# Kernel optimization log

Hardware: AMD Instinct MI355X
Metric: run time of the kernel (lower is better)

Reference implementation:

```python
import jax, jax.numpy as jnp
import numpy as np

B, E, H, KVH, S = 1, 4096, 32, 8, 2048
HD = E // H            # per-head dim = 128
KVE = KVH * HD         # kv projection embed dim = 1024


def setup_inputs() -> dict:
    key = jax.random.key(0)
    ks = jax.random.split(key, 10)
    std = 0.02
    return {
        "input_embeds": jax.random.normal(ks[0], (B, E, 1, S), jnp.float32),
        "cos": jax.random.uniform(ks[1], (HD, S), jnp.float32, -1.0, 1.0),
        "sin": jax.random.uniform(ks[2], (HD, S), jnp.float32, -1.0, 1.0),
        "wq": jax.random.normal(ks[3], (E, E), jnp.float32) * std,
        "bq": jnp.zeros((E,), jnp.float32),
        "wk": jax.random.normal(ks[4], (KVE, E), jnp.float32) * std,
        "wv": jax.random.normal(ks[5], (KVE, E), jnp.float32) * std,
        "bv": jnp.zeros((KVE,), jnp.float32),
        "wo": jax.random.normal(ks[6], (E, E), jnp.float32) * std,
        "bo": jnp.zeros((E,), jnp.float32),
    }


def _proj(w, x, b=None):
    # 1x1 Conv2d == channelwise linear on (B, C, 1, S)
    y = jnp.einsum('oc,bcxs->boxs', w, x)
    if b is not None:
        y = y + b[None, :, None, None]
    return y


def _rope(x, cos, sin):
    # x: (B, h, HD, S); rotate-half along head_dim axis
    half = x.shape[2] // 2
    x1, x2 = x[:, :, :half], x[:, :, half:]
    rot = jnp.concatenate([-x2, x1], axis=2)
    return x * cos[None, None] + rot * sin[None, None]


def reference(input_embeds, cos, sin, wq, bq, wk, wv, bv, wo, bo):
    b, e, _, s = input_embeds.shape
    hd = e // H
    q = _proj(wq, input_embeds, bq)          # (B, E, 1, S)
    k = _proj(wk, input_embeds)              # (B, KVE, 1, S)  (no bias)
    v = _proj(wv, input_embeds, bv)          # (B, KVE, 1, S)

    qh = q.reshape(b, H, hd, s)
    kh = k.reshape(b, KVH, hd, s)
    qh = _rope(qh, cos, sin)
    kh = _rope(kh, cos, sin)

    # GQA tiling: channel-block repeat => query head h uses kv head (h % KVH)
    rep = H // KVH
    kfull = jnp.tile(kh, (1, rep, 1, 1))                       # (B, H, HD, S)
    vfull = jnp.tile(v.reshape(b, KVH, hd, s), (1, rep, 1, 1))  # (B, H, HD, S)

    scale = 1.0 / np.sqrt(hd).astype(np.float32)
    scores = jnp.einsum('bhcq,bhck->bhqk', qh, kfull) * scale  # (B, H, S, S)
    causal = jnp.tril(jnp.ones((s, s), bool))
    scores = jnp.where(causal[None, None], scores, jnp.finfo(scores.dtype).min)
    w = jax.nn.softmax(scores, axis=-1)
    attn = jnp.einsum('bhqk,bhck->bhcq', w, vfull).reshape(b, e, 1, s)
    return _proj(wo, attn, bo)
```

## Files before the change

### kernel.cpp

```cpp
#include <hip/hip_runtime.h>


typedef unsigned short u16;
typedef unsigned int u32;
typedef __attribute__((ext_vector_type(8))) short bf16x8;
typedef __attribute__((ext_vector_type(4))) float f32x4;

__device__ __forceinline__ u16 f2b(float f){
  union { float f; u32 u; } v; v.f = f;
  u32 r = (v.u + 0x7FFFu + ((v.u >> 16) & 1u)) >> 16;
  return (u16)r;
}
__device__ __forceinline__ float b2f(u16 b){
  union { u32 u; float f; } v; v.u = ((u32)b) << 16;
  return v.f;
}

__device__ __forceinline__ void gld16(const void* g, void* l){
  __builtin_amdgcn_global_load_lds((const __attribute__((address_space(1))) u32*)g,
                                   (__attribute__((address_space(3))) u32*)l, 16, 0, 0);
}

__global__ __launch_bounds__(256) void cvt_w(const float* __restrict__ src,
                                             u16* __restrict__ dst, int n4)
{
  int i = blockIdx.x * 256 + threadIdx.x;
  if (i < n4){
    float4 v = *(const float4*)&src[(size_t)i * 4];
    ushort4 o; o.x = f2b(v.x); o.y = f2b(v.y); o.z = f2b(v.z); o.w = f2b(v.w);
    *(ushort4*)&dst[(size_t)i * 4] = o;
  }
}

__global__ __launch_bounds__(256) void transpose_x(const float* __restrict__ X,
                                                   u16* __restrict__ XT)
{
  __shared__ float lds[64][65];
  const int c0 = blockIdx.x * 64, s0 = blockIdx.y * 64;
  const int tid = threadIdx.x;
  {
    const int sg = tid & 15, cl = tid >> 4;
#pragma unroll
    for (int p = 0; p < 4; ++p){
      int c = cl + p * 16;
      float4 v = *(const float4*)&X[(size_t)(c0 + c) * 2048 + s0 + sg * 4];
      lds[sg*4+0][c] = v.x; lds[sg*4+1][c] = v.y;
      lds[sg*4+2][c] = v.z; lds[sg*4+3][c] = v.w;
    }
  }
  __syncthreads();
  {
    const int cg = tid & 15, sl = tid >> 4;
#pragma unroll
    for (int p = 0; p < 4; ++p){
      int s = sl + p * 16;
      ushort4 o;
      o.x = f2b(lds[s][cg*4+0]); o.y = f2b(lds[s][cg*4+1]);
      o.z = f2b(lds[s][cg*4+2]); o.w = f2b(lds[s][cg*4+3]);
      *(ushort4*)&XT[(size_t)(s0 + s) * 4096 + c0 + cg * 4] = o;
    }
  }
}

template<int EPI, int ABF>
__global__ __launch_bounds__(256) void gemm2(
    const u16* __restrict__ W0, const u16* __restrict__ W1, const u16* __restrict__ W2,
    const float* __restrict__ F0, const float* __restrict__ F1, const float* __restrict__ F2,
    const u16* __restrict__ B,
    const float* __restrict__ bias0, const float* __restrict__ bias2,
    u16* __restrict__ QTo, u16* __restrict__ KTo, u16* __restrict__ Vno,
    float* __restrict__ OUT)
{
  const int K = 4096;
  const int m0 = blockIdx.y * 128, n0 = blockIdx.x * 128;

  const u16* A16; const float* Af; int mA;
  if (EPI == 0){
    if (m0 < 4096)      { A16 = W0; Af = F0; mA = m0; }
    else if (m0 < 5120) { A16 = W1; Af = F1; mA = m0 - 4096; }
    else                { A16 = W2; Af = F2; mA = m0 - 5120; }
  } else { A16 = W0; Af = F0; mA = m0; }

  __shared__ __align__(16) u16 As[128 * 32];
  __shared__ __align__(16) u16 Bs[128 * 32];

  const int tid = threadIdx.x, lane = tid & 63, w = tid >> 6;
  const int wm = w >> 1, wn = w & 1, quad = lane >> 4, l15 = lane & 15;

  f32x4 acc[4][4];
#pragma unroll
  for (int mt = 0; mt < 4; ++mt)
#pragma unroll
    for (int nt = 0; nt < 4; ++nt)
      acc[mt][nt] = f32x4{0.f, 0.f, 0.f, 0.f};

  const int r0 = tid >> 2, gs0 = tid & 3;
  const int g0 = gs0 ^ ((r0 >> 1) & 3);
  const int r1 = r0 + 64;

  u16* ldsA0 = As + (size_t)(w * 64) * 8;
  u16* ldsA1 = As + (size_t)(w * 64 + 256) * 8;
  u16* ldsB0 = Bs + (size_t)(w * 64) * 8;
  u16* ldsB1 = Bs + (size_t)(w * 64 + 256) * 8;

  const u16* bsrc0 = &B[(size_t)(n0 + r0) * 4096 + g0 * 8];
  const u16* bsrc1 = &B[(size_t)(n0 + r1) * 4096 + g0 * 8];
  const u16* asrc0 = ABF ? &A16[(size_t)(mA + r0) * 4096 + g0 * 8] : nullptr;
  const u16* asrc1 = ABF ? &A16[(size_t)(mA + r1) * 4096 + g0 * 8] : nullptr;
  const float* afs0 = ABF ? nullptr : &Af[(size_t)(mA + r0) * 4096 + g0 * 8];
  const float* afs1 = ABF ? nullptr : &Af[(size_t)(mA + r1) * 4096 + g0 * 8];

  int aoff[4], boff[4];
#pragma unroll
  for (int mt = 0; mt < 4; ++mt){
    int row = wm * 64 + mt * 16 + l15;
    aoff[mt] = row * 32 + (quad ^ ((row >> 1) & 3)) * 8;
  }
#pragma unroll
  for (int nt = 0; nt < 4; ++nt){
    int row = wn * 64 + nt * 16 + l15;
    boff[nt] = row * 32 + (quad ^ ((row >> 1) & 3)) * 8;
  }

  for (int kt = 0; kt < K / 32; ++kt){
    const int k0 = kt * 32;
    if (ABF){
      gld16(asrc0 + k0, ldsA0);
      gld16(asrc1 + k0, ldsA1);
    } else {
      float4 v0 = *(const float4*)&afs0[k0];
      float4 v1 = *(const float4*)&afs0[k0 + 4];
      float4 v2 = *(const float4*)&afs1[k0];
      float4 v3 = *(const float4*)&afs1[k0 + 4];
      union { u16 u[8]; uint4 q; } p0, p1;
      p0.u[0]=f2b(v0.x); p0.u[1]=f2b(v0.y); p0.u[2]=f2b(v0.z); p0.u[3]=f2b(v0.w);
      p0.u[4]=f2b(v1.x); p0.u[5]=f2b(v1.y); p0.u[6]=f2b(v1.z); p0.u[7]=f2b(v1.w);
      p1.u[0]=f2b(v2.x); p1.u[1]=f2b(v2.y); p1.u[2]=f2b(v2.z); p1.u[3]=f2b(v2.w);
      p1.u[4]=f2b(v3.x); p1.u[5]=f2b(v3.y); p1.u[6]=f2b(v3.z); p1.u[7]=f2b(v3.w);
      *(uint4*)&As[(size_t)tid * 8] = p0.q;
      *(uint4*)&As[(size_t)(tid + 256) * 8] = p1.q;
    }
    gld16(bsrc0 + k0, ldsB0);
    gld16(bsrc1 + k0, ldsB1);
    __syncthreads();

    bf16x8 af[4], bfr[4];
#pragma unroll
    for (int mt = 0; mt < 4; ++mt) af[mt]  = *(const bf16x8*)&As[aoff[mt]];
#pragma unroll
    for (int nt = 0; nt < 4; ++nt) bfr[nt] = *(const bf16x8*)&Bs[boff[nt]];
#pragma unroll
    for (int mt = 0; mt < 4; ++mt)
#pragma unroll
      for (int nt = 0; nt < 4; ++nt)
        acc[mt][nt] = __builtin_amdgcn_mfma_f32_16x16x32_bf16(af[mt], bfr[nt], acc[mt][nt], 0, 0, 0);
    __syncthreads();
  }

  if (EPI == 0){
    if (m0 < 4096){
#pragma unroll
      for (int mt = 0; mt < 4; ++mt){
        int mb = m0 + wm * 64 + mt * 16 + quad * 4;
        float b0 = bias0[mb], b1 = bias0[mb+1], b2 = bias0[mb+2], b3 = bias0[mb+3];
#pragma unroll
        for (int nt = 0; nt < 4; ++nt){
          int n = n0 + wn * 64 + nt * 16 + l15;
          ushort4 o;
          o.x = f2b(acc[mt][nt][0] + b0); o.y = f2b(acc[mt][nt][1] + b1);
          o.z = f2b(acc[mt][nt][2] + b2); o.w = f2b(acc[mt][nt][3] + b3);
          *(ushort4*)&QTo[(size_t)n * 4096 + mb] = o;
        }
      }
    } else if (m0 < 5120){
#pragma unroll
      for (int mt = 0; mt < 4; ++mt){
        int mb = m0 - 4096 + wm * 64 + mt * 16 + quad * 4;
#pragma unroll
        for (int nt = 0; nt < 4; ++nt){
          int n = n0 + wn * 64 + nt * 16 + l15;
          ushort4 o;
          o.x = f2b(acc[mt][nt][0]); o.y = f2b(acc[mt][nt][1]);
          o.z = f2b(acc[mt][nt][2]); o.w = f2b(acc[mt][nt][3]);
          *(ushort4*)&KTo[(size_t)n * 1024 + mb] = o;
        }
      }
    } else {
#pragma unroll
      for (int mt = 0; mt < 4; ++mt)
#pragma unroll
        for (int r = 0; r < 4; ++r){
          int mv = m0 - 5120 + wm * 64 + mt * 16 + quad * 4 + r;
          float bb = bias2[mv];
#pragma unroll
          for (int nt = 0; nt < 4; ++nt){
            int n = n0 + wn * 64 + nt * 16 + l15;
            Vno[(size_t)mv * 2048 + n] = f2b(acc[mt][nt][r] + bb);
          }
        }
    }
  } else {
#pragma unroll
    for (int mt = 0; mt < 4; ++mt)
#pragma unroll
      for (int r = 0; r < 4; ++r){
        int m = m0 + wm * 64 + mt * 16 + quad * 4 + r;
        float bb = bias0[m];
#pragma unroll
        for (int nt = 0; nt < 4; ++nt){
          int n = n0 + wn * 64 + nt * 16 + l15;
          OUT[(size_t)m * 2048 + n] = acc[mt][nt][r] + bb;
        }
      }
  }
}

template<int EPI>
__global__ __launch_bounds__(512, 2) void gemm256(
    const u16* __restrict__ W0, const u16* __restrict__ W1, const u16* __restrict__ W2,
    const u16* __restrict__ Bmat,
    const float* __restrict__ bias0, const float* __restrict__ bias2,
    u16* __restrict__ QTo, u16* __restrict__ KTo, u16* __restrict__ Vno,
    float* __restrict__ OUT)
{
  const int NT = 64;
  const int m0 = blockIdx.y * 256, n0 = blockIdx.x * 256;

  const u16* A16; int mA;
  if (EPI == 0){
    if (m0 < 4096)      { A16 = W0; mA = m0; }
    else if (m0 < 5120) { A16 = W1; mA = m0 - 4096; }
    else                { A16 = W2; mA = m0 - 5120; }
  } else { A16 = W0; mA = m0; }

  __shared__ __align__(16) u16 As[2 * 2 * 8192];
  __shared__ __align__(16) u16 Bs[2 * 2 * 8192];

  const int tid = threadIdx.x, lane = tid & 63, w = tid >> 6;
  const int wm = w >> 2, wn = w & 3, quad = lane >> 4, l15 = lane & 15;

  f32x4 acc[8][4];
#pragma unroll
  for (int mt = 0; mt < 8; ++mt)
#pragma unroll
    for (int nt = 0; nt < 4; ++nt)
      acc[mt][nt] = f32x4{0.f, 0.f, 0.f, 0.f};

  const int rowq = tid >> 2;
  const int kg   = (tid & 3) * 8;
  const u16* aG = &A16[(size_t)(mA + rowq) * 4096 + kg];
  const u16* bG = &Bmat[(size_t)(n0 + rowq) * 4096 + kg];
  u16* AsW = As + w * 512;
  u16* BsW = Bs + w * 512;

  int aoff[8], boff[4];
#pragma unroll
  for (int mt = 0; mt < 8; ++mt) aoff[mt] = (wm * 128 + mt * 16 + l15) * 32 + quad * 8;
#pragma unroll
  for (int nt = 0; nt < 4; ++nt) boff[nt] = (wn * 64 + nt * 16 + l15) * 32 + quad * 8;

  auto stage8 = [&](int b, int k0){
    u16* Ad = AsW + b * 16384;
    u16* Bd = BsW + b * 16384;
    const u16* as_ = aG + k0;
    const u16* bs_ = bG + k0;
    gld16(as_,                   Ad);
    gld16(as_ + 128 * 4096,      Ad + 4096);
    gld16(bs_,                   Bd);
    gld16(bs_ + 128 * 4096,      Bd + 4096);
    gld16(as_ + 32,              Ad + 8192);
    gld16(as_ + 32 + 128 * 4096, Ad + 8192 + 4096);
    gld16(bs_ + 32,              Bd + 8192);
    gld16(bs_ + 32 + 128 * 4096, Bd + 8192 + 4096);
  };

  stage8(0, 0);
  asm volatile("s_waitcnt vmcnt(4)" ::: "memory");
  __builtin_amdgcn_s_barrier();
  __builtin_amdgcn_sched_barrier(0);

#pragma unroll 1
  for (int t = 0; t < NT; ++t){
    const int buf = t & 1;
    const u16* Asl = As + buf * 16384;
    const u16* Bsl = Bs + buf * 16384;

    {
      bf16x8 af[8], bf[4];
#pragma unroll
      for (int mt = 0; mt < 8; ++mt) af[mt] = *(const bf16x8*)&Asl[aoff[mt]];
#pragma unroll
      for (int nt = 0; nt < 4; ++nt) bf[nt] = *(const bf16x8*)&Bsl[boff[nt]];
      if (t + 1 < NT) stage8((t + 1) & 1, (t + 1) * 64);
      __builtin_amdgcn_s_setprio(1);
#pragma unroll
      for (int mt = 0; mt < 8; ++mt)
#pragma unroll
        for (int nt = 0; nt < 4; ++nt)
          acc[mt][nt] = __builtin_amdgcn_mfma_f32_16x16x32_bf16(af[mt], bf[nt], acc[mt][nt], 0, 0, 0);
      __builtin_amdgcn_s_setprio(0);
      if (t + 1 < NT) { asm volatile("s_waitcnt vmcnt(8)" ::: "memory"); }
      else            { asm volatile("s_waitcnt vmcnt(0)" ::: "memory"); }
      __builtin_amdgcn_s_barrier();
      __builtin_amdgcn_sched_barrier(0);
    }
    {
      bf16x8 af[8], bf[4];
#pragma unroll
      for (int mt = 0; mt < 8; ++mt) af[mt] = *(const bf16x8*)&Asl[8192 + aoff[mt]];
#pragma unroll
      for (int nt = 0; nt < 4; ++nt) bf[nt] = *(const bf16x8*)&Bsl[8192 + boff[nt]];
      __builtin_amdgcn_s_setprio(1);
#pragma unroll
      for (int mt = 0; mt < 8; ++mt)
#pragma unroll
        for (int nt = 0; nt < 4; ++nt)
          acc[mt][nt] = __builtin_amdgcn_mfma_f32_16x16x32_bf16(af[mt], bf[nt], acc[mt][nt], 0, 0, 0);
      __builtin_amdgcn_s_setprio(0);
      if (t + 1 < NT) { asm volatile("s_waitcnt vmcnt(4)" ::: "memory"); }
      __builtin_amdgcn_s_barrier();
      __builtin_amdgcn_sched_barrier(0);
    }
  }

  if (EPI == 0){
    if (m0 < 4096){
#pragma unroll
      for (int mt = 0; mt < 8; ++mt){
        int mb = m0 + wm * 128 + mt * 16 + quad * 4;
        float b0 = bias0[mb], b1 = bias0[mb+1], b2 = bias0[mb+2], b3 = bias0[mb+3];
#pragma unroll
        for (int nt = 0; nt < 4; ++nt){
          int n = n0 + wn * 64 + nt * 16 + l15;
          ushort4 o;
          o.x = f2b(acc[mt][nt][0] + b0); o.y = f2b(acc[mt][nt][1] + b1);
          o.z = f2b(acc[mt][nt][2] + b2); o.w = f2b(acc[mt][nt][3] + b3);
          *(ushort4*)&QTo[(size_t)n * 4096 + mb] = o;
        }
      }
    } else if (m0 < 5120){
#pragma unroll
      for (int mt = 0; mt < 8; ++mt){
        int mb = m0 - 4096 + wm * 128 + mt * 16 + quad * 4;
#pragma unroll
        for (int nt = 0; nt < 4; ++nt){
          int n = n0 + wn * 64 + nt * 16 + l15;
          ushort4 o;
          o.x = f2b(acc[mt][nt][0]); o.y = f2b(acc[mt][nt][1]);
          o.z = f2b(acc[mt][nt][2]); o.w = f2b(acc[mt][nt][3]);
          *(ushort4*)&KTo[(size_t)n * 1024 + mb] = o;
        }
      }
    } else {
#pragma unroll
      for (int mt = 0; mt < 8; ++mt)
#pragma unroll
        for (int r = 0; r < 4; ++r){
          int mv = m0 - 5120 + wm * 128 + mt * 16 + quad * 4 + r;
          float bb = bias2[mv];
#pragma unroll
          for (int nt = 0; nt < 4; ++nt){
            int n = n0 + wn * 64 + nt * 16 + l15;
            Vno[(size_t)mv * 2048 + n] = f2b(acc[mt][nt][r] + bb);
          }
        }
    }
  } else {
#pragma unroll
    for (int mt = 0; mt < 8; ++mt)
#pragma unroll
      for (int r = 0; r < 4; ++r){
        int m = m0 + wm * 128 + mt * 16 + quad * 4 + r;
        float bb = bias0[m];
#pragma unroll
        for (int nt = 0; nt < 4; ++nt){
          int n = n0 + wn * 64 + nt * 16 + l15;
          OUT[(size_t)m * 2048 + n] = acc[mt][nt][r] + bb;
        }
      }
  }
}

__global__ __launch_bounds__(256) void rope_kernel(u16* __restrict__ QT,
                                                   u16* __restrict__ KT,
                                                   const float* __restrict__ cosp,
                                                   const float* __restrict__ sinp)
{
  const float qscale = 0.08838834764831845f * 1.4426950408889634f;
  int gid = blockIdx.x * 256 + threadIdx.x;
  const int NQ = 2048 * 32 * 64;
  if (gid < NQ){
    int c = gid & 63, hh = (gid >> 6) & 31, s = gid >> 11;
    size_t base = (size_t)s * 4096 + hh * 128 + c;
    float x1 = b2f(QT[base]), x2 = b2f(QT[base + 64]);
    float c1 = cosp[c * 2048 + s],        s1 = sinp[c * 2048 + s];
    float c2 = cosp[(c + 64) * 2048 + s], s2 = sinp[(c + 64) * 2048 + s];
    QT[base]      = f2b((x1 * c1 - x2 * s1) * qscale);
    QT[base + 64] = f2b((x2 * c2 + x1 * s2) * qscale);
  } else {
    int g = gid - NQ;
    int c = g & 63, hh = (g >> 6) & 7, s = g >> 9;
    size_t base = (size_t)s * 1024 + hh * 128 + c;
    float x1 = b2f(KT[base]), x2 = b2f(KT[base + 64]);
    float c1 = cosp[c * 2048 + s],        s1 = sinp[c * 2048 + s];
    float c2 = cosp[(c + 64) * 2048 + s], s2 = sinp[(c + 64) * 2048 + s];
    KT[base]      = f2b(x1 * c1 - x2 * s1);
    KT[base + 64] = f2b(x2 * c2 + x1 * s2);
  }
}

__global__ __launch_bounds__(256, 1) void attn3(const u16* __restrict__ QT,
                                                const u16* __restrict__ KT,
                                                const u16* __restrict__ Vn,
                                                u16* __restrict__ AT)
{
  const int h = blockIdx.x;
  const int p = blockIdx.y;
  const int kvh = h & 7;
  const int tid = threadIdx.x;
  const int w = tid >> 6, lane = tid & 63;
  const int quad = lane >> 4, l15 = lane & 15;

  const int k  = 4 * p + w;
  const int t1 = k, t2 = 63 - k;
  const int e1 = t1 >> 1, e2 = t2 >> 1;
  const int i01 = t1 * 32, i02 = t2 * 32;
  const int U = 32 - 2 * p;

  __shared__ __align__(16) u16 Ks[2][64 * 128];
  __shared__ __align__(16) u16 Vs[128 * 64];
  __shared__ __align__(16) u16 Ps[4][16][64];

  bf16x8 qa1[2][4], qa2[2][4];
#pragma unroll
  for (int mt = 0; mt < 2; ++mt)
#pragma unroll
    for (int kc = 0; kc < 4; ++kc){
      qa1[mt][kc] = *(const bf16x8*)&QT[(size_t)(i01 + mt * 16 + l15) * 4096
                                        + h * 128 + kc * 32 + quad * 8];
      qa2[mt][kc] = *(const bf16x8*)&QT[(size_t)(i02 + mt * 16 + l15) * 4096
                                        + h * 128 + kc * 32 + quad * 8];
    }

  f32x4 o1[2][9], o2[2][9];
#pragma unroll
  for (int mt = 0; mt < 2; ++mt)
#pragma unroll
    for (int ct = 0; ct < 9; ++ct){
      o1[mt][ct] = f32x4{0.f, 0.f, 0.f, 0.f};
      o2[mt][ct] = f32x4{0.f, 0.f, 0.f, 0.f};
    }

  bf16x8 ones;
#pragma unroll
  for (int z = 0; z < 8; ++z) ones[z] = (short)0x3F80;

  const int krl = lane >> 4, kgl = lane & 15;
  const int vrl = lane >> 3, vgl = lane & 7;

  auto stageK = [&](int buf, int j0){
#pragma unroll
    for (int q = 0; q < 4; ++q){
      int r = w * 16 + q * 4 + krl;
      gld16(&KT[(size_t)(j0 + r) * 1024 + kvh * 128 + ((kgl ^ (r & 7)) * 8)],
            &Ks[buf][(size_t)(w * 16 + q * 4) * 128]);
    }
  };
  auto stageV = [&](int j0){
#pragma unroll
    for (int q = 0; q < 4; ++q){
      int r = w * 32 + q * 8 + vrl;
      gld16(&Vn[(size_t)(kvh * 128 + r) * 2048 + j0 + ((vgl ^ (r & 7)) * 8)],
            &Vs[(size_t)(w * 32 + q * 8) * 64]);
    }
  };

  auto soft = [&](f32x4 (&s)[2][4], bf16x8 (&pa)[2][2], f32x4 (&o)[2][9],
                  int i0, int j0, bool maskit){
#pragma unroll
    for (int mt = 0; mt < 2; ++mt){
#pragma unroll
      for (int nt = 0; nt < 4; ++nt)
#pragma unroll
        for (int r = 0; r < 4; ++r){
          float pv = exp2f(fminf(s[mt][nt][r], 60.0f));
          if (maskit && (j0 + nt * 16 + l15 > i0 + mt * 16 + quad * 4 + r)) pv = 0.0f;
          int col = nt * 16 + l15, rowp = quad * 4 + r;
          Ps[w][rowp][((col >> 3) ^ (rowp & 7)) * 8 + (col & 7)] = f2b(pv);
        }
#pragma unroll
      for (int kc = 0; kc < 2; ++kc){
        pa[mt][kc] = *(const bf16x8*)&Ps[w][l15][((kc * 4 + quad) ^ (l15 & 7)) * 8];
        o[mt][8] = __builtin_amdgcn_mfma_f32_16x16x32_bf16(pa[mt][kc], ones, o[mt][8], 0, 0, 0);
      }
    }
  };

  auto epilogue = [&](f32x4 (&o)[2][9], int i0){
#pragma unroll
    for (int mt = 0; mt < 2; ++mt){
      float rinv[4];
#pragma unroll
      for (int r = 0; r < 4; ++r) rinv[r] = 1.0f / o[mt][8][r];
#pragma unroll
      for (int ct = 0; ct < 8; ++ct)
#pragma unroll
        for (int r = 0; r < 4; ++r){
          int i = i0 + mt * 16 + quad * 4 + r;
          AT[(size_t)i * 4096 + h * 128 + ct * 16 + l15] = f2b(o[mt][ct][r] * rinv[r]);
        }
    }
  };

  stageK(0, 0);
  for (int u = 0; u < U; ++u){
    __syncthreads();
    if (u + 1 < U) stageK((u + 1) & 1, (u + 1) * 64);
    stageV(u * 64);

    const int j0 = u * 64;
    const bool act1 = (u <= e1), act2 = (u <= e2);
    const u16* Kb = &Ks[u & 1][0];

    f32x4 s1[2][4], s2[2][4];
    bf16x8 pa1[2][2], pa2[2][2];
    if (act2 || act1){
#pragma unroll
      for (int mt = 0; mt < 2; ++mt)
#pragma unroll
        for (int nt = 0; nt < 4; ++nt){
          s1[mt][nt] = f32x4{0.f, 0.f, 0.f, 0.f};
          s2[mt][nt] = f32x4{0.f, 0.f, 0.f, 0.f};
        }
#pragma unroll
      for (int nt = 0; nt < 4; ++nt){
        bf16x8 kb[4];
#pragma unroll
        for (int kc = 0; kc < 4; ++kc){
          int row = nt * 16 + l15;
          kb[kc] = *(const bf16x8*)&Kb[row * 128 + (((kc * 4 + quad) ^ (row & 7)) * 8)];
        }
#pragma unroll
        for (int kc = 0; kc < 4; ++kc){
          s2[0][nt] = __builtin_amdgcn_mfma_f32_16x16x32_bf16(qa2[0][kc], kb[kc], s2[0][nt], 0, 0, 0);
          s2[1][nt] = __builtin_amdgcn_mfma_f32_16x16x32_bf16(qa2[1][kc], kb[kc], s2[1][nt], 0, 0, 0);
        }
        if (act1)
#pragma unroll
          for (int kc = 0; kc < 4; ++kc){
            s1[0][nt] = __builtin_amdgcn_mfma_f32_16x16x32_bf16(qa1[0][kc], kb[kc], s1[0][nt], 0, 0, 0);
            s1[1][nt] = __builtin_amdgcn_mfma_f32_16x16x32_bf16(qa1[1][kc], kb[kc], s1[1][nt], 0, 0, 0);
          }
      }
      if (act2) soft(s2, pa2, o2, i02, j0, u == e2);
      if (act1) soft(s1, pa1, o1, i01, j0, u == e1);
    }
    __syncthreads();

    if (act2 || act1){
#pragma unroll
      for (int ct = 0; ct < 8; ++ct)
#pragma unroll
        for (int kc = 0; kc < 2; ++kc){
          int row = ct * 16 + l15;
          bf16x8 vb = *(const bf16x8*)&Vs[row * 64 + (((kc * 4 + quad) ^ (row & 7)) * 8)];
          if (act2){
            o2[0][ct] = __builtin_amdgcn_mfma_f32_16x16x32_bf16(pa2[0][kc], vb, o2[0][ct], 0, 0, 0);
            o2[1][ct] = __builtin_amdgcn_mfma_f32_16x16x32_bf16(pa2[1][kc], vb, o2[1][ct], 0, 0, 0);
          }
          if (act1){
            o1[0][ct] = __builtin_amdgcn_mfma_f32_16x16x32_bf16(pa1[0][kc], vb, o1[0][ct], 0, 0, 0);
            o1[1][ct] = __builtin_amdgcn_mfma_f32_16x16x32_bf16(pa1[1][kc], vb, o1[1][ct], 0, 0, 0);
          }
        }
      if (u == e2) epilogue(o2, i02);
      if (u == e1) epilogue(o1, i01);
    }
  }
}

extern "C" void kernel_launch(void* const* d_in, const int* in_sizes, int n_in,
                              void* d_out, int out_size, void* d_ws, size_t ws_size,
                              hipStream_t stream)
{
  const float* X    = (const float*)d_in[0];
  const float* cosp = (const float*)d_in[1];
  const float* sinp = (const float*)d_in[2];
  const float* wq   = (const float*)d_in[3];
  const float* bq   = (const float*)d_in[4];
  const float* wk   = (const float*)d_in[5];
  const float* wv   = (const float*)d_in[6];
  const float* bv   = (const float*)d_in[7];
  const float* wo   = (const float*)d_in[8];
  const float* bo   = (const float*)d_in[9];
  float* out = (float*)d_out;

  char* ws = (char*)d_ws;
  const size_t MB = 1u << 20;

  if (ws_size >= 88 * MB){
    u16* W16Q = (u16*)(ws);
    u16* W16K = (u16*)(ws + 32 * MB);
    u16* W16V = (u16*)(ws + 40 * MB);
    u16* XT   = (u16*)(ws + 48 * MB);
    u16* QT   = (u16*)(ws + 64 * MB);
    u16* KT   = (u16*)(ws + 80 * MB);
    u16* Vn   = (u16*)(ws + 84 * MB);
    u16* AT   = (u16*)(ws + 48 * MB);
    u16* WO16 = (u16*)(ws);

    cvt_w<<<16384, 256, 0, stream>>>(wq, W16Q, 4194304);
    cvt_w<<< 4096, 256, 0, stream>>>(wk, W16K, 1048576);
    cvt_w<<< 4096, 256, 0, stream>>>(wv, W16V, 1048576);
    transpose_x<<<dim3(64, 32), 256, 0, stream>>>(X, XT);
    gemm256<0><<<dim3(8, 24), 512, 0, stream>>>(W16Q, W16K, W16V, XT,
                                                bq, bv, QT, KT, Vn, nullptr);
    cvt_w<<<16384, 256, 0, stream>>>(wo, WO16, 4194304);
    rope_kernel<<<20480, 256, 0, stream>>>(QT, KT, cosp, sinp);
    attn3<<<dim3(32, 8), 256, 0, stream>>>(QT, KT, Vn, AT);
    gemm256<1><<<dim3(8, 16), 512, 0, stream>>>(WO16, nullptr, nullptr, AT,
                                                bo, nullptr, nullptr, nullptr, nullptr, out);
  } else {
    u16* XT = (u16*)(ws);
    u16* QT = (u16*)(ws + 16 * MB);
    u16* KT = (u16*)(ws + 32 * MB);
    u16* Vn = (u16*)(ws + 36 * MB);
    u16* AT = (u16*)(ws + 40 * MB);

    transpose_x<<<dim3(64, 32), 256, 0, stream>>>(X, XT);
    gemm2<0,0><<<dim3(16, 48), 256, 0, stream>>>(nullptr, nullptr, nullptr, wq, wk, wv,
                                                 XT, bq, bv, QT, KT, Vn, nullptr);
    rope_kernel<<<20480, 256, 0, stream>>>(QT, KT, cosp, sinp);
    attn3<<<dim3(32, 8), 256, 0, stream>>>(QT, KT, Vn, AT);
    gemm2<1,0><<<dim3(16, 32), 256, 0, stream>>>(nullptr, nullptr, nullptr, wo, nullptr, nullptr,
                                                 AT, bo, nullptr, nullptr, nullptr, nullptr, out);
  }
}
```

Before: 673.1 us.

## Split attention work so each wave owns one query tile, doubling grid

The causal attention kernel previously had each wave process two paired query tiles (t and 63-t) within 8 blocks per head. Now each block handles a pair of block-rows q and 15-q. Two waves take consecutive early tiles and two take consecutive late tiles, with one tile per wave, giving 512 blocks instead of 256. This raises occupancy and parallelism across the CUs and halves per-wave register state. In exchange, each K/V tile is staged by more blocks and waves within a block are less balanced.

```diff
diff --git a/kernel.cpp b/kernel.cpp
--- a/kernel.cpp
+++ b/kernel.cpp
@@ -409,47 +409,42 @@
   }
 }
 
-__global__ __launch_bounds__(256, 1) void attn3(const u16* __restrict__ QT,
+__global__ __launch_bounds__(256, 1) void attn4(const u16* __restrict__ QT,
                                                 const u16* __restrict__ KT,
                                                 const u16* __restrict__ Vn,
                                                 u16* __restrict__ AT)
 {
   const int h = blockIdx.x;
-  const int p = blockIdx.y;
+  const int Y = blockIdx.y;
+  const int q = (Y < 8) ? Y : 23 - Y;
   const int kvh = h & 7;
   const int tid = threadIdx.x;
   const int w = tid >> 6, lane = tid & 63;
   const int quad = lane >> 4, l15 = lane & 15;
 
-  const int k  = 4 * p + w;
-  const int t1 = k, t2 = 63 - k;
-  const int e1 = t1 >> 1, e2 = t2 >> 1;
-  const int i01 = t1 * 32, i02 = t2 * 32;
-  const int U = 32 - 2 * p;
+  const int t = (w < 2) ? (2 * q + w) : (62 - 2 * q + (w - 2));
+  const int e  = t >> 1;
+  const int i0 = t * 32;
+  const int U  = 32 - q;
 
   __shared__ __align__(16) u16 Ks[2][64 * 128];
   __shared__ __align__(16) u16 Vs[128 * 64];
   __shared__ __align__(16) u16 Ps[4][16][64];
 
-  bf16x8 qa1[2][4], qa2[2][4];
+  bf16x8 qa[2][4];
 #pragma unroll
   for (int mt = 0; mt < 2; ++mt)
 #pragma unroll
-    for (int kc = 0; kc < 4; ++kc){
-      qa1[mt][kc] = *(const bf16x8*)&QT[(size_t)(i01 + mt * 16 + l15) * 4096
-                                        + h * 128 + kc * 32 + quad * 8];
-      qa2[mt][kc] = *(const bf16x8*)&QT[(size_t)(i02 + mt * 16 + l15) * 4096
-                                        + h * 128 + kc * 32 + quad * 8];
-    }
-
-  f32x4 o1[2][9], o2[2][9];
+    for (int kc = 0; kc < 4; ++kc)
+      qa[mt][kc] = *(const bf16x8*)&QT[(size_t)(i0 + mt * 16 + l15) * 4096
+                                       + h * 128 + kc * 32 + quad * 8];
+
+  f32x4 o[2][9];
 #pragma unroll
   for (int mt = 0; mt < 2; ++mt)
 #pragma unroll
-    for (int ct = 0; ct < 9; ++ct){
-      o1[mt][ct] = f32x4{0.f, 0.f, 0.f, 0.f};
-      o2[mt][ct] = f32x4{0.f, 0.f, 0.f, 0.f};
-    }
+    for (int ct = 0; ct < 9; ++ct)
+      o[mt][ct] = f32x4{0.f, 0.f, 0.f, 0.f};
 
   bf16x8 ones;
 #pragma unroll
@@ -460,55 +455,18 @@
 
   auto stageK = [&](int buf, int j0){
 #pragma unroll
-    for (int q = 0; q < 4; ++q){
-      int r = w * 16 + q * 4 + krl;
+    for (int qq = 0; qq < 4; ++qq){
+      int r = w * 16 + qq * 4 + krl;
       gld16(&KT[(size_t)(j0 + r) * 1024 + kvh * 128 + ((kgl ^ (r & 7)) * 8)],
-            &Ks[buf][(size_t)(w * 16 + q * 4) * 128]);
+            &Ks[buf][(size_t)(w * 16 + qq * 4) * 128]);
     }
   };
   auto stageV = [&](int j0){
 #pragma unroll
-    for (int q = 0; q < 4; ++q){
-      int r = w * 32 + q * 8 + vrl;
+    for (int qq = 0; qq < 4; ++qq){
+      int r = w * 32 + qq * 8 + vrl;
       gld16(&Vn[(size_t)(kvh * 128 + r) * 2048 + j0 + ((vgl ^ (r & 7)) * 8)],
-            &Vs[(size_t)(w * 32 + q * 8) * 64]);
-    }
-  };
-
-  auto soft = [&](f32x4 (&s)[2][4], bf16x8 (&pa)[2][2], f32x4 (&o)[2][9],
-                  int i0, int j0, bool maskit){
-#pragma unroll
-    for (int mt = 0; mt < 2; ++mt){
-#pragma unroll
-      for (int nt = 0; nt < 4; ++nt)
-#pragma unroll
-        for (int r = 0; r < 4; ++r){
-          float pv = exp2f(fminf(s[mt][nt][r], 60.0f));
-          if (maskit && (j0 + nt * 16 + l15 > i0 + mt * 16 + quad * 4 + r)) pv = 0.0f;
-          int col = nt * 16 + l15, rowp = quad * 4 + r;
-          Ps[w][rowp][((col >> 3) ^ (rowp & 7)) * 8 + (col & 7)] = f2b(pv);
-        }
-#pragma unroll
-      for (int kc = 0; kc < 2; ++kc){
-        pa[mt][kc] = *(const bf16x8*)&Ps[w][l15][((kc * 4 + quad) ^ (l15 & 7)) * 8];
-        o[mt][8] = __builtin_amdgcn_mfma_f32_16x16x32_bf16(pa[mt][kc], ones, o[mt][8], 0, 0, 0);
-      }
-    }
-  };
-
-  auto epilogue = [&](f32x4 (&o)[2][9], int i0){
-#pragma unroll
-    for (int mt = 0; mt < 2; ++mt){
-      float rinv[4];
-#pragma unroll
-      for (int r = 0; r < 4; ++r) rinv[r] = 1.0f / o[mt][8][r];
-#pragma unroll
-      for (int ct = 0; ct < 8; ++ct)
-#pragma unroll
-        for (int r = 0; r < 4; ++r){
-          int i = i0 + mt * 16 + quad * 4 + r;
-          AT[(size_t)i * 4096 + h * 128 + ct * 16 + l15] = f2b(o[mt][ct][r] * rinv[r]);
-        }
+            &Vs[(size_t)(w * 32 + qq * 8) * 64]);
     }
   };
 
@@ -519,19 +477,17 @@
     stageV(u * 64);
 
     const int j0 = u * 64;
-    const bool act1 = (u <= e1), act2 = (u <= e2);
+    const bool act = (u <= e);
     const u16* Kb = &Ks[u & 1][0];
 
-    f32x4 s1[2][4], s2[2][4];
-    bf16x8 pa1[2][2], pa2[2][2];
-    if (act2 || act1){
+    f32x4 s[2][4];
+    bf16x8 pa[2][2];
+    if (act){
 #pragma unroll
       for (int mt = 0; mt < 2; ++mt)
 #pragma unroll
-        for (int nt = 0; nt < 4; ++nt){
-          s1[mt][nt] = f32x4{0.f, 0.f, 0.f, 0.f};
-          s2[mt][nt] = f32x4{0.f, 0.f, 0.f, 0.f};
-        }
+        for (int nt = 0; nt < 4; ++nt)
+          s[mt][nt] = f32x4{0.f, 0.f, 0.f, 0.f};
 #pragma unroll
       for (int nt = 0; nt < 4; ++nt){
         bf16x8 kb[4];
@@ -542,39 +498,56 @@
         }
 #pragma unroll
         for (int kc = 0; kc < 4; ++kc){
-          s2[0][nt] = __builtin_amdgcn_mfma_f32_16x16x32_bf16(qa2[0][kc], kb[kc], s2[0][nt], 0, 0, 0);
-          s2[1][nt] = __builtin_amdgcn_mfma_f32_16x16x32_bf16(qa2[1][kc], kb[kc], s2[1][nt], 0, 0, 0);
-        }
-        if (act1)
-#pragma unroll
-          for (int kc = 0; kc < 4; ++kc){
-            s1[0][nt] = __builtin_amdgcn_mfma_f32_16x16x32_bf16(qa1[0][kc], kb[kc], s1[0][nt], 0, 0, 0);
-            s1[1][nt] = __builtin_amdgcn_mfma_f32_16x16x32_bf16(qa1[1][kc], kb[kc], s1[1][nt], 0, 0, 0);
+          s[0][nt] = __builtin_amdgcn_mfma_f32_16x16x32_bf16(qa[0][kc], kb[kc], s[0][nt], 0, 0, 0);
+          s[1][nt] = __builtin_amdgcn_mfma_f32_16x16x32_bf16(qa[1][kc], kb[kc], s[1][nt], 0, 0, 0);
+        }
+      }
+      const bool maskit = (u == e);
+#pragma unroll
+      for (int mt = 0; mt < 2; ++mt){
+#pragma unroll
+        for (int nt = 0; nt < 4; ++nt)
+#pragma unroll
+          for (int r = 0; r < 4; ++r){
+            float pv = exp2f(fminf(s[mt][nt][r], 60.0f));
+            if (maskit && (j0 + nt * 16 + l15 > i0 + mt * 16 + quad * 4 + r)) pv = 0.0f;
+            int col = nt * 16 + l15, rowp = quad * 4 + r;
+            Ps[w][rowp][((col >> 3) ^ (rowp & 7)) * 8 + (col & 7)] = f2b(pv);
           }
-      }
-      if (act2) soft(s2, pa2, o2, i02, j0, u == e2);
-      if (act1) soft(s1, pa1, o1, i01, j0, u == e1);
+#pragma unroll
+        for (int kc = 0; kc < 2; ++kc){
+          pa[mt][kc] = *(const bf16x8*)&Ps[w][l15][((kc * 4 + quad) ^ (l15 & 7)) * 8];
+          o[mt][8] = __builtin_amdgcn_mfma_f32_16x16x32_bf16(pa[mt][kc], ones, o[mt][8], 0, 0, 0);
+        }
+      }
     }
     __syncthreads();
 
-    if (act2 || act1){
+    if (act){
 #pragma unroll
       for (int ct = 0; ct < 8; ++ct)
 #pragma unroll
         for (int kc = 0; kc < 2; ++kc){
           int row = ct * 16 + l15;
           bf16x8 vb = *(const bf16x8*)&Vs[row * 64 + (((kc * 4 + quad) ^ (row & 7)) * 8)];
-          if (act2){
-            o2[0][ct] = __builtin_amdgcn_mfma_f32_16x16x32_bf16(pa2[0][kc], vb, o2[0][ct], 0, 0, 0);
-            o2[1][ct] = __builtin_amdgcn_mfma_f32_16x16x32_bf16(pa2[1][kc], vb, o2[1][ct], 0, 0, 0);
-          }
-          if (act1){
-            o1[0][ct] = __builtin_amdgcn_mfma_f32_16x16x32_bf16(pa1[0][kc], vb, o1[0][ct], 0, 0, 0);
-            o1[1][ct] = __builtin_amdgcn_mfma_f32_16x16x32_bf16(pa1[1][kc], vb, o1[1][ct], 0, 0, 0);
-          }
-        }
-      if (u == e2) epilogue(o2, i02);
-      if (u == e1) epilogue(o1, i01);
+          o[0][ct] = __builtin_amdgcn_mfma_f32_16x16x32_bf16(pa[0][kc], vb, o[0][ct], 0, 0, 0);
+          o[1][ct] = __builtin_amdgcn_mfma_f32_16x16x32_bf16(pa[1][kc], vb, o[1][ct], 0, 0, 0);
+        }
+      if (u == e){
+#pragma unroll
+        for (int mt = 0; mt < 2; ++mt){
+          float rinv[4];
+#pragma unroll
+          for (int r = 0; r < 4; ++r) rinv[r] = 1.0f / o[mt][8][r];
+#pragma unroll
+          for (int ct = 0; ct < 8; ++ct)
+#pragma unroll
+            for (int r = 0; r < 4; ++r){
+              int i = i0 + mt * 16 + quad * 4 + r;
+              AT[(size_t)i * 4096 + h * 128 + ct * 16 + l15] = f2b(o[mt][ct][r] * rinv[r]);
+            }
+        }
+      }
     }
   }
 }
@@ -617,7 +590,7 @@
                                                 bq, bv, QT, KT, Vn, nullptr);
     cvt_w<<<16384, 256, 0, stream>>>(wo, WO16, 4194304);
     rope_kernel<<<20480, 256, 0, stream>>>(QT, KT, cosp, sinp);
-    attn3<<<dim3(32, 8), 256, 0, stream>>>(QT, KT, Vn, AT);
+    attn4<<<dim3(32, 16), 256, 0, stream>>>(QT, KT, Vn, AT);
     gemm256<1><<<dim3(8, 16), 512, 0, stream>>>(WO16, nullptr, nullptr, AT,
                                                 bo, nullptr, nullptr, nullptr, nullptr, out);
   } else {
@@ -631,7 +604,7 @@
     gemm2<0,0><<<dim3(16, 48), 256, 0, stream>>>(nullptr, nullptr, nullptr, wq, wk, wv,
                                                  XT, bq, bv, QT, KT, Vn, nullptr);
     rope_kernel<<<20480, 256, 0, stream>>>(QT, KT, cosp, sinp);
-    attn3<<<dim3(32, 8), 256, 0, stream>>>(QT, KT, Vn, AT);
+    attn4<<<dim3(32, 16), 256, 0, stream>>>(QT, KT, Vn, AT);
     gemm2<1,0><<<dim3(16, 32), 256, 0, stream>>>(nullptr, nullptr, nullptr, wo, nullptr, nullptr,
                                                  AT, bo, nullptr, nullptr, nullptr, nullptr, out);
   }
```

Result: no change. 676.9 us (+0.6%).
